# Kernel tuning notes

Measured on AMD Instinct MI355X. Metric: run time of the kernel, lower is better.

Reference implementation:

```python
import jax, jax.numpy as jnp
import numpy as np


def conv1x1(x, W, b):
    # x: [B, Cin, H, W], W: [Cout, Cin], b: [Cout] -> [B, Cout, H, W]
    return jnp.einsum('bchw,oc->bohw', x, W) + b[None, :, None, None]


def setup_inputs() -> dict:
    key = jax.random.key(0)
    ks = jax.random.split(key, 10)
    B, C, H, W = 16, 512, 64, 64
    c = C // 8  # in_ch // scale
    s_in = 1.0 / np.sqrt(C)
    s_c = 1.0 / np.sqrt(c)
    return {
        'x': jax.random.normal(ks[0], (B, C, H, W), dtype=jnp.float32),
        'Wq': jax.random.normal(ks[1], (c, C), dtype=jnp.float32) * s_in,
        'bq': jax.random.normal(ks[2], (c,), dtype=jnp.float32) * 0.01,
        'Wk': jax.random.normal(ks[3], (c, C), dtype=jnp.float32) * s_in,
        'bk': jax.random.normal(ks[4], (c,), dtype=jnp.float32) * 0.01,
        'Wv': jax.random.normal(ks[5], (c, C), dtype=jnp.float32) * s_in,
        'bv': jax.random.normal(ks[6], (c,), dtype=jnp.float32) * 0.01,
        'Wo': jax.random.normal(ks[7], (C, c), dtype=jnp.float32) * s_c,
        'bo': jax.random.normal(ks[8], (C,), dtype=jnp.float32) * 0.01,
        'gamma': jax.random.uniform(ks[9], (1,), dtype=jnp.float32),
    }


def reference(x, Wq, bq, Wk, bk, Wv, bv, Wo, bo, gamma):
    B, C, H, W = x.shape
    c = Wq.shape[0]
    N = H * W
    queries = conv1x1(x, Wq, bq).reshape(B, c, N)          # [B, c, N]
    # NOTE: original torch code does .view(-1, h*w, c): a pure reshape of the
    # contiguous [B, c, N] buffer, NOT a transpose. Reproduce exactly.
    keys = conv1x1(x, Wk, bk).reshape(B, N, c)             # [B, N, c] (reshape!)
    attn = jax.nn.softmax(jnp.einsum('bcn,bnd->bcd', queries, keys), axis=-1)  # [B, c, c]
    values = conv1x1(x, Wv, bv).reshape(B, c, N)           # [B, c, N]
    out = jnp.einsum('bcd,bdn->bcn', attn, values).reshape(B, c, H, W)
    out = conv1x1(out, Wo, bo)                             # [B, C, H, W]
    return out * gamma + x
```

## Files before the change

kernel.cpp:

```cpp
#include <hip/hip_runtime.h>

typedef unsigned short ushortT;
typedef unsigned int uintT;
typedef __attribute__((ext_vector_type(8))) short short8;
typedef __attribute__((ext_vector_type(4))) float float4v;

constexpr int B  = 16;
constexpr int C  = 512;
constexpr int CC = 64;
constexpr int N  = 4096;

constexpr size_t QK_OFF  = 0;
constexpr size_t S_OFF   = 8388608;
constexpr size_t VT_OFF  = 8454144;
constexpr size_t MF_OFF  = 10551296;
constexpr size_t WH_OFF  = 10813440;
constexpr size_t WL_OFF  = 10862592;
constexpr size_t WOT_OFF = 10911744;

#define GLL(lds, g) __builtin_amdgcn_global_load_lds( \
    (const __attribute__((address_space(1))) void*)(g), \
    (__attribute__((address_space(3))) void*)(lds), 16, 0, 0)

static __device__ __forceinline__ ushortT f2bf(float f) {
    uintT u = __float_as_uint(f);
    u = (u + 0x7fffu + ((u >> 16) & 1u)) >> 16;
    return (ushortT)u;
}
static __device__ __forceinline__ float bf2f(ushortT h) {
    return __uint_as_float(((uintT)h) << 16);
}

__global__ __launch_bounds__(256) void k_prep_w(
    const float* __restrict__ Wq, const float* __restrict__ Wk,
    const float* __restrict__ Wv, const float* __restrict__ Wo,
    ushortT* __restrict__ wh, ushortT* __restrict__ wl, float* __restrict__ wot)
{
    int idx = blockIdx.x * 256 + threadIdx.x;
    if (idx < 3 * CC * C) {
        int m = idx >> 9, k = idx & 511;
        const float* W = (m < 64) ? Wq : (m < 128 ? Wk : Wv);
        float v = W[(m & 63) * C + k];
        ushortT h = f2bf(v);
        ushortT l = f2bf(v - bf2f(h));
        int kt = k >> 6, kk = k & 63;
        size_t off = ((size_t)(kt * 192 + m)) * 64 + (size_t)(((kk >> 3) ^ (m & 7)) * 8) + (kk & 7);
        wh[off] = h;
        wl[off] = l;
    } else {
        int i2 = idx - 3 * CC * C;
        int cc = i2 >> 9, co = i2 & 511;
        wot[i2] = Wo[co * CC + cc];
    }
}

__global__ __launch_bounds__(256) void k_qkv(
    const float* __restrict__ x,
    const ushortT* __restrict__ wh, const ushortT* __restrict__ wl,
    const float* __restrict__ bq, const float* __restrict__ bk,
    const float* __restrict__ bv,
    float* __restrict__ qk, ushortT* __restrict__ vt)
{
    __shared__ ushortT As[192 * 64];
    __shared__ ushortT Bh[64 * 64];
    __shared__ ushortT Bl[64 * 64];

    const int tid  = threadIdx.x;
    const int n0   = blockIdx.x * 64;
    const int b    = blockIdx.y;
    const int lane = tid & 63;
    const int wv   = tid >> 6;
    const int L15  = lane & 15, Lq = lane >> 4;

    const int nl    = tid & 63;
    const int kbase = tid >> 6;

    float4v acc[3][4];
    const float4v vzero = {0.f, 0.f, 0.f, 0.f};
#pragma unroll
    for (int mi = 0; mi < 3; ++mi)
#pragma unroll
        for (int ni = 0; ni < 4; ++ni) acc[mi][ni] = vzero;

    for (int kt = 0; kt < 8; ++kt) {
        const float* xs = x + ((size_t)(b * C + kt * 64)) * N + n0 + nl;
#pragma unroll
        for (int it = 0; it < 16; ++it) {
            int kk = kbase + it * 4;
            float v = xs[(size_t)kk * N];
            ushortT h = f2bf(v);
            ushortT l = f2bf(v - bf2f(h));
            int idx = nl * 64 + (((kk >> 3) ^ (nl & 7)) * 8) + (kk & 7);
            Bh[idx] = h;
            Bl[idx] = l;
        }
        {
            const char* src = (const char*)wh + (size_t)kt * 24576;
#pragma unroll
            for (int i = 0; i < 6; ++i) {
                int off = i * 4096 + tid * 16;
                GLL((char*)As + off, src + off);
            }
        }
        __syncthreads();
#pragma unroll
        for (int s = 0; s < 2; ++s) {
            short8 fbh[4], fbl[4];
#pragma unroll
            for (int ni = 0; ni < 4; ++ni) {
                int row = ni * 16 + L15;
                int off = row * 64 + ((4 * s + Lq) ^ (row & 7)) * 8;
                fbh[ni] = *(const short8*)&Bh[off];
                fbl[ni] = *(const short8*)&Bl[off];
            }
#pragma unroll
            for (int mi = 0; mi < 3; ++mi) {
                int rm = 48 * wv + mi * 16 + L15;
                short8 a = *(const short8*)&As[rm * 64 + (((4 * s + Lq) ^ (rm & 7)) * 8)];
#pragma unroll
                for (int ni = 0; ni < 4; ++ni)
                    acc[mi][ni] = __builtin_amdgcn_mfma_f32_16x16x32_bf16(a, fbh[ni], acc[mi][ni], 0, 0, 0);
#pragma unroll
                for (int ni = 0; ni < 4; ++ni)
                    acc[mi][ni] = __builtin_amdgcn_mfma_f32_16x16x32_bf16(a, fbl[ni], acc[mi][ni], 0, 0, 0);
            }
        }
        __syncthreads();
        {
            const char* src = (const char*)wl + (size_t)kt * 24576;
#pragma unroll
            for (int i = 0; i < 6; ++i) {
                int off = i * 4096 + tid * 16;
                GLL((char*)As + off, src + off);
            }
        }
        __syncthreads();
#pragma unroll
        for (int s = 0; s < 2; ++s) {
            short8 fbh[4];
#pragma unroll
            for (int ni = 0; ni < 4; ++ni) {
                int row = ni * 16 + L15;
                fbh[ni] = *(const short8*)&Bh[row * 64 + ((4 * s + Lq) ^ (row & 7)) * 8];
            }
#pragma unroll
            for (int mi = 0; mi < 3; ++mi) {
                int rm = 48 * wv + mi * 16 + L15;
                short8 a = *(const short8*)&As[rm * 64 + (((4 * s + Lq) ^ (rm & 7)) * 8)];
#pragma unroll
                for (int ni = 0; ni < 4; ++ni)
                    acc[mi][ni] = __builtin_amdgcn_mfma_f32_16x16x32_bf16(a, fbh[ni], acc[mi][ni], 0, 0, 0);
            }
        }
        __syncthreads();
    }

#pragma unroll
    for (int mi = 0; mi < 3; ++mi) {
        int rbase = 48 * wv + mi * 16;
        int type = rbase >> 6;
#pragma unroll
        for (int ni = 0; ni < 4; ++ni) {
            int col = n0 + ni * 16 + L15;
            float4v v4 = acc[mi][ni];
#pragma unroll
            for (int reg = 0; reg < 4; ++reg) {
                int rl = (rbase + Lq * 4 + reg) & 63;
                float val = v4[reg];
                if (type == 0) {
                    qk[((size_t)(b * 64 + rl)) * N + col] = val + bq[rl];
                } else if (type == 1) {
                    qk[((size_t)((16 + b) * 64 + rl)) * N + col] = val + bk[rl];
                } else {
                    ushortT bb = f2bf(val + bv[rl]);
                    size_t off = ((size_t)(b * N + col)) * 64 + (((rl >> 3) ^ (col & 7)) * 8) + (rl & 7);
                    vt[off] = bb;
                }
            }
        }
    }
}

__global__ __launch_bounds__(256) void k_logits(
    const float* __restrict__ qk, float* __restrict__ S)
{
    int b  = blockIdx.x;
    int n0 = blockIdx.y * 64;
    __shared__ float Qs[64 * 68];
    __shared__ float Ks[64 * 64];

    const float* Qb = qk + (size_t)b * (CC * N);
    const float* Kb = qk + (size_t)(16 + b) * (CC * N);
    int tid = threadIdx.x;

    for (int t = tid; t < 64 * 64; t += 256) {
        int i = t >> 6, nn = t & 63;
        Qs[i * 68 + nn] = Qb[(size_t)i * N + n0 + nn];
        Ks[t] = Kb[(size_t)n0 * 64 + t];
    }
    __syncthreads();

    int ti = tid >> 4, tj = tid & 15;
    int i0 = ti * 4, j0 = tj * 4;
    float accl[4][4] = {};
    for (int nn = 0; nn < 64; ++nn) {
        float4 kv = *reinterpret_cast<const float4*>(&Ks[nn * 64 + j0]);
        float qa[4];
#pragma unroll
        for (int a = 0; a < 4; ++a) qa[a] = Qs[(i0 + a) * 68 + nn];
#pragma unroll
        for (int a = 0; a < 4; ++a) {
            accl[a][0] = fmaf(qa[a], kv.x, accl[a][0]);
            accl[a][1] = fmaf(qa[a], kv.y, accl[a][1]);
            accl[a][2] = fmaf(qa[a], kv.z, accl[a][2]);
            accl[a][3] = fmaf(qa[a], kv.w, accl[a][3]);
        }
    }
    float* Sb = S + b * (CC * CC);
#pragma unroll
    for (int a = 0; a < 4; ++a)
#pragma unroll
        for (int bb = 0; bb < 4; ++bb)
            atomicAdd(&Sb[(i0 + a) * 64 + j0 + bb], accl[a][bb]);
}

__global__ __launch_bounds__(256) void k_softmax_m(
    const float* __restrict__ S, const float* __restrict__ wot,
    ushortT* __restrict__ mf)
{
    int b = blockIdx.x, chunk = blockIdx.y;
    __shared__ float A[64 * 65];
    int tid = threadIdx.x;
    const float* Sb = S + b * (CC * CC);

    for (int t = tid; t < 4096; t += 256) A[(t >> 6) * 65 + (t & 63)] = Sb[t];
    __syncthreads();
    if (tid < 64) {
        float mx = -1e30f;
        for (int j = 0; j < 64; ++j) mx = fmaxf(mx, A[tid * 65 + j]);
        float sum = 0.f;
        for (int j = 0; j < 64; ++j) {
            float e = __expf(A[tid * 65 + j] - mx);
            A[tid * 65 + j] = e;
            sum += e;
        }
        float inv = 1.f / sum;
        for (int j = 0; j < 64; ++j) A[tid * 65 + j] *= inv;
    }
    __syncthreads();

    int co = chunk * 64 + (tid & 63);
    int e0 = (tid >> 6) * 16;
    float acc[16] = {};
    for (int cc = 0; cc < 64; ++cc) {
        float w = wot[cc * C + co];
#pragma unroll
        for (int ee = 0; ee < 16; ++ee)
            acc[ee] = fmaf(w, A[cc * 65 + e0 + ee], acc[ee]);
    }
#pragma unroll
    for (int d = 0; d < 2; ++d) {
        int c = (e0 >> 3) + d;
        uintT p0 = (uintT)f2bf(acc[d * 8 + 0]) | ((uintT)f2bf(acc[d * 8 + 1]) << 16);
        uintT p1 = (uintT)f2bf(acc[d * 8 + 2]) | ((uintT)f2bf(acc[d * 8 + 3]) << 16);
        uintT p2 = (uintT)f2bf(acc[d * 8 + 4]) | ((uintT)f2bf(acc[d * 8 + 5]) << 16);
        uintT p3 = (uintT)f2bf(acc[d * 8 + 6]) | ((uintT)f2bf(acc[d * 8 + 7]) << 16);
        uint4 pk = make_uint4(p0, p1, p2, p3);
        size_t off = ((size_t)(b * C + co)) * 64 + (size_t)((c ^ (co & 7)) * 8);
        *(uint4*)&mf[off] = pk;
    }
}

__global__ __launch_bounds__(256) void k_out(
    const ushortT* __restrict__ vt, const ushortT* __restrict__ mf,
    const float* __restrict__ x, const float* __restrict__ bo,
    const float* __restrict__ gamma, float* __restrict__ out)
{
    __shared__ ushortT As[64 * 64];
    __shared__ ushortT Bs[256 * 64];

    int b = blockIdx.x, ct = blockIdx.y, nt = blockIdx.z;
    int co0 = ct * 64, n0 = nt * 256;
    int tid = threadIdx.x;
    const char* asrc = (const char*)mf + ((size_t)(b * C + co0)) * 128;
    const char* bsrc = (const char*)vt + ((size_t)(b * N + n0)) * 128;
#pragma unroll
    for (int i = 0; i < 2; ++i) {
        int off = i * 4096 + tid * 16;
        GLL((char*)As + off, asrc + off);
    }
#pragma unroll
    for (int i = 0; i < 8; ++i) {
        int off = i * 4096 + tid * 16;
        GLL((char*)Bs + off, bsrc + off);
    }
    __syncthreads();

    int lane = tid & 63, wv = tid >> 6;
    int L15 = lane & 15, Lq = lane >> 4;
    float4v acc[4][4];
    const float4v vzero = {0.f, 0.f, 0.f, 0.f};
#pragma unroll
    for (int mi = 0; mi < 4; ++mi)
#pragma unroll
        for (int ni = 0; ni < 4; ++ni) acc[mi][ni] = vzero;

#pragma unroll
    for (int s = 0; s < 2; ++s) {
        short8 fb[4];
#pragma unroll
        for (int ni = 0; ni < 4; ++ni) {
            int row = wv * 64 + ni * 16 + L15;
            fb[ni] = *(const short8*)&Bs[row * 64 + ((4 * s + Lq) ^ (row & 7)) * 8];
        }
#pragma unroll
        for (int mi = 0; mi < 4; ++mi) {
            int rm = mi * 16 + L15;
            short8 a = *(const short8*)&As[rm * 64 + ((4 * s + Lq) ^ (rm & 7)) * 8];
#pragma unroll
            for (int ni = 0; ni < 4; ++ni)
                acc[mi][ni] = __builtin_amdgcn_mfma_f32_16x16x32_bf16(a, fb[ni], acc[mi][ni], 0, 0, 0);
        }
    }

    float g = gamma[0];
#pragma unroll
    for (int mi = 0; mi < 4; ++mi) {
        int cob = co0 + mi * 16 + Lq * 4;
#pragma unroll
        for (int ni = 0; ni < 4; ++ni) {
            int col = n0 + wv * 64 + ni * 16 + L15;
            float4v v4 = acc[mi][ni];
#pragma unroll
            for (int reg = 0; reg < 4; ++reg) {
                int c2 = cob + reg;
                size_t idx = ((size_t)(b * C + c2)) * N + col;
                out[idx] = fmaf(g, v4[reg] + bo[c2], x[idx]);
            }
        }
    }
}

extern "C" void kernel_launch(void* const* d_in, const int* in_sizes, int n_in,
                              void* d_out, int out_size, void* d_ws, size_t ws_size,
                              hipStream_t stream)
{
    const float* x     = (const float*)d_in[0];
    const float* Wq    = (const float*)d_in[1];
    const float* bq    = (const float*)d_in[2];
    const float* Wk    = (const float*)d_in[3];
    const float* bk    = (const float*)d_in[4];
    const float* Wv    = (const float*)d_in[5];
    const float* bv    = (const float*)d_in[6];
    const float* Wo    = (const float*)d_in[7];
    const float* bo    = (const float*)d_in[8];
    const float* gamma = (const float*)d_in[9];

    float* ws   = (float*)d_ws;
    float* qk   = ws + QK_OFF;
    float* S    = ws + S_OFF;
    ushortT* vt = (ushortT*)(ws + VT_OFF);
    ushortT* mf = (ushortT*)(ws + MF_OFF);
    ushortT* wh = (ushortT*)(ws + WH_OFF);
    ushortT* wl = (ushortT*)(ws + WL_OFF);
    float* wot  = ws + WOT_OFF;

    hipMemsetAsync(S, 0, (size_t)B * CC * CC * sizeof(float), stream);
    k_prep_w<<<512, 256, 0, stream>>>(Wq, Wk, Wv, Wo, wh, wl, wot);
    k_qkv<<<dim3(64, 16), 256, 0, stream>>>(x, wh, wl, bq, bk, bv, qk, vt);
    k_logits<<<dim3(16, 64), 256, 0, stream>>>(qk, S);
    k_softmax_m<<<dim3(16, 8), 256, 0, stream>>>(S, wot, mf);
    k_out<<<dim3(16, 8, 16), 256, 0, stream>>>(vt, mf, x, bo, gamma, (float*)d_out);
}
```

Measured before the change: 420.0 us.

## Double-buffer QKV projection, coarsen logits blocks, vectorize output epilogues

The QKV projection kernel now keeps the high and low weight halves in LDS together and double-buffers the split x tile. It prefetches the next k-tile's x into registers while the current tile runs its MFMAs, and merges the two MFMA passes into one loop with a single barrier pair. The logits kernel processes four N-chunks per block with float4 loads, which cuts atomic traffic by a factor of four, and the V store is packed into 4-element vectors. The output kernel swaps the MFMA operand roles so each lane holds contiguous spatial elements, enabling float4 loads of x and float4 stores of out. These changes cost extra LDS and registers per block, which may lower occupancy.

```diff
diff --git a/kernel.cpp b/kernel.cpp
--- a/kernel.cpp
+++ b/kernel.cpp
@@ -3,6 +3,7 @@
 typedef unsigned short ushortT;
 typedef unsigned int uintT;
 typedef __attribute__((ext_vector_type(8))) short short8;
+typedef __attribute__((ext_vector_type(4))) short short4v;
 typedef __attribute__((ext_vector_type(4))) float float4v;
 
 constexpr int B  = 16;
@@ -61,9 +62,10 @@
     const float* __restrict__ bv,
     float* __restrict__ qk, ushortT* __restrict__ vt)
 {
-    __shared__ ushortT As[192 * 64];
-    __shared__ ushortT Bh[64 * 64];
-    __shared__ ushortT Bl[64 * 64];
+    __shared__ ushortT Ah[192 * 64];
+    __shared__ ushortT Al[192 * 64];
+    __shared__ ushortT Bh[2][64 * 64];
+    __shared__ ushortT Bl[2][64 * 64];
 
     const int tid  = threadIdx.x;
     const int n0   = blockIdx.x * 64;
@@ -72,9 +74,12 @@
     const int wv   = tid >> 6;
     const int L15  = lane & 15, Lq = lane >> 4;
 
-    const int nl    = tid & 63;
-    const int kbase = tid >> 6;
-
+    const int nl  = tid & 63;
+    const int kg0 = tid >> 6;
+
+    const float* xb = x + (size_t)b * C * N + n0 + nl;
+
+    float xr[2][8];
     float4v acc[3][4];
     const float4v vzero = {0.f, 0.f, 0.f, 0.f};
 #pragma unroll
@@ -82,27 +87,51 @@
 #pragma unroll
         for (int ni = 0; ni < 4; ++ni) acc[mi][ni] = vzero;
 
+#pragma unroll
+    for (int u = 0; u < 2; ++u) {
+        const int kg = kg0 + 4 * u;
+#pragma unroll
+        for (int j = 0; j < 8; ++j)
+            xr[u][j] = xb[(size_t)(kg * 8 + j) * N];
+    }
+    {
+        const char* srcH = (const char*)wh;
+        const char* srcL = (const char*)wl;
+#pragma unroll
+        for (int i = 0; i < 6; ++i) {
+            int off = i * 4096 + tid * 16;
+            GLL((char*)Ah + off, srcH + off);
+            GLL((char*)Al + off, srcL + off);
+        }
+    }
+#pragma unroll
+    for (int u = 0; u < 2; ++u) {
+        const int kg = kg0 + 4 * u;
+        short8 h8, l8;
+#pragma unroll
+        for (int j = 0; j < 8; ++j) {
+            float v = xr[u][j];
+            ushortT h = f2bf(v);
+            h8[j] = (short)h;
+            l8[j] = (short)f2bf(v - bf2f(h));
+        }
+        int idx = nl * 64 + (kg ^ (nl & 7)) * 8;
+        *(short8*)&Bh[0][idx] = h8;
+        *(short8*)&Bl[0][idx] = l8;
+    }
+    __syncthreads();
+
     for (int kt = 0; kt < 8; ++kt) {
-        const float* xs = x + ((size_t)(b * C + kt * 64)) * N + n0 + nl;
-#pragma unroll
-        for (int it = 0; it < 16; ++it) {
-            int kk = kbase + it * 4;
-            float v = xs[(size_t)kk * N];
-            ushortT h = f2bf(v);
-            ushortT l = f2bf(v - bf2f(h));
-            int idx = nl * 64 + (((kk >> 3) ^ (nl & 7)) * 8) + (kk & 7);
-            Bh[idx] = h;
-            Bl[idx] = l;
-        }
-        {
-            const char* src = (const char*)wh + (size_t)kt * 24576;
-#pragma unroll
-            for (int i = 0; i < 6; ++i) {
-                int off = i * 4096 + tid * 16;
-                GLL((char*)As + off, src + off);
-            }
-        }
-        __syncthreads();
+        const int cur = kt & 1;
+        if (kt < 7) {
+#pragma unroll
+            for (int u = 0; u < 2; ++u) {
+                const int kg = kg0 + 4 * u;
+#pragma unroll
+                for (int j = 0; j < 8; ++j)
+                    xr[u][j] = xb[(size_t)((kt + 1) * 64 + kg * 8 + j) * N];
+            }
+        }
 #pragma unroll
         for (int s = 0; s < 2; ++s) {
             short8 fbh[4], fbl[4];
@@ -110,49 +139,54 @@
             for (int ni = 0; ni < 4; ++ni) {
                 int row = ni * 16 + L15;
                 int off = row * 64 + ((4 * s + Lq) ^ (row & 7)) * 8;
-                fbh[ni] = *(const short8*)&Bh[off];
-                fbl[ni] = *(const short8*)&Bl[off];
+                fbh[ni] = *(const short8*)&Bh[cur][off];
+                fbl[ni] = *(const short8*)&Bl[cur][off];
             }
 #pragma unroll
             for (int mi = 0; mi < 3; ++mi) {
                 int rm = 48 * wv + mi * 16 + L15;
-                short8 a = *(const short8*)&As[rm * 64 + (((4 * s + Lq) ^ (rm & 7)) * 8)];
+                int aoff = rm * 64 + ((4 * s + Lq) ^ (rm & 7)) * 8;
+                short8 ah = *(const short8*)&Ah[aoff];
+                short8 al = *(const short8*)&Al[aoff];
 #pragma unroll
                 for (int ni = 0; ni < 4; ++ni)
-                    acc[mi][ni] = __builtin_amdgcn_mfma_f32_16x16x32_bf16(a, fbh[ni], acc[mi][ni], 0, 0, 0);
+                    acc[mi][ni] = __builtin_amdgcn_mfma_f32_16x16x32_bf16(ah, fbh[ni], acc[mi][ni], 0, 0, 0);
 #pragma unroll
                 for (int ni = 0; ni < 4; ++ni)
-                    acc[mi][ni] = __builtin_amdgcn_mfma_f32_16x16x32_bf16(a, fbl[ni], acc[mi][ni], 0, 0, 0);
+                    acc[mi][ni] = __builtin_amdgcn_mfma_f32_16x16x32_bf16(al, fbh[ni], acc[mi][ni], 0, 0, 0);
+#pragma unroll
+                for (int ni = 0; ni < 4; ++ni)
+                    acc[mi][ni] = __builtin_amdgcn_mfma_f32_16x16x32_bf16(ah, fbl[ni], acc[mi][ni], 0, 0, 0);
             }
         }
         __syncthreads();
-        {
-            const char* src = (const char*)wl + (size_t)kt * 24576;
+        if (kt < 7) {
+            const char* srcH = (const char*)wh + (size_t)(kt + 1) * 24576;
+            const char* srcL = (const char*)wl + (size_t)(kt + 1) * 24576;
 #pragma unroll
             for (int i = 0; i < 6; ++i) {
                 int off = i * 4096 + tid * 16;
-                GLL((char*)As + off, src + off);
-            }
-        }
-        __syncthreads();
-#pragma unroll
-        for (int s = 0; s < 2; ++s) {
-            short8 fbh[4];
-#pragma unroll
-            for (int ni = 0; ni < 4; ++ni) {
-                int row = ni * 16 + L15;
-                fbh[ni] = *(const short8*)&Bh[row * 64 + ((4 * s + Lq) ^ (row & 7)) * 8];
-            }
-#pragma unroll
-            for (int mi = 0; mi < 3; ++mi) {
-                int rm = 48 * wv + mi * 16 + L15;
-                short8 a = *(const short8*)&As[rm * 64 + (((4 * s + Lq) ^ (rm & 7)) * 8)];
-#pragma unroll
-                for (int ni = 0; ni < 4; ++ni)
-                    acc[mi][ni] = __builtin_amdgcn_mfma_f32_16x16x32_bf16(a, fbh[ni], acc[mi][ni], 0, 0, 0);
-            }
-        }
-        __syncthreads();
+                GLL((char*)Ah + off, srcH + off);
+                GLL((char*)Al + off, srcL + off);
+            }
+            const int nxt = cur ^ 1;
+#pragma unroll
+            for (int u = 0; u < 2; ++u) {
+                const int kg = kg0 + 4 * u;
+                short8 h8, l8;
+#pragma unroll
+                for (int j = 0; j < 8; ++j) {
+                    float v = xr[u][j];
+                    ushortT h = f2bf(v);
+                    h8[j] = (short)h;
+                    l8[j] = (short)f2bf(v - bf2f(h));
+                }
+                int idx = nl * 64 + (kg ^ (nl & 7)) * 8;
+                *(short8*)&Bh[nxt][idx] = h8;
+                *(short8*)&Bl[nxt][idx] = l8;
+            }
+            __syncthreads();
+        }
     }
 
 #pragma unroll
@@ -163,19 +197,26 @@
         for (int ni = 0; ni < 4; ++ni) {
             int col = n0 + ni * 16 + L15;
             float4v v4 = acc[mi][ni];
-#pragma unroll
-            for (int reg = 0; reg < 4; ++reg) {
-                int rl = (rbase + Lq * 4 + reg) & 63;
-                float val = v4[reg];
-                if (type == 0) {
-                    qk[((size_t)(b * 64 + rl)) * N + col] = val + bq[rl];
-                } else if (type == 1) {
-                    qk[((size_t)((16 + b) * 64 + rl)) * N + col] = val + bk[rl];
-                } else {
-                    ushortT bb = f2bf(val + bv[rl]);
-                    size_t off = ((size_t)(b * N + col)) * 64 + (((rl >> 3) ^ (col & 7)) * 8) + (rl & 7);
-                    vt[off] = bb;
+            if (type == 0) {
+#pragma unroll
+                for (int reg = 0; reg < 4; ++reg) {
+                    int rl = (rbase + Lq * 4 + reg) & 63;
+                    qk[((size_t)(b * 64 + rl)) * N + col] = v4[reg] + bq[rl];
                 }
+            } else if (type == 1) {
+#pragma unroll
+                for (int reg = 0; reg < 4; ++reg) {
+                    int rl = (rbase + Lq * 4 + reg) & 63;
+                    qk[((size_t)((16 + b) * 64 + rl)) * N + col] = v4[reg] + bk[rl];
+                }
+            } else {
+                int rl0 = (rbase + Lq * 4) & 63;
+                short4v p;
+#pragma unroll
+                for (int reg = 0; reg < 4; ++reg)
+                    p[reg] = (short)f2bf(v4[reg] + bv[rl0 + reg]);
+                size_t off = ((size_t)(b * N + col)) * 64 + (size_t)(((rl0 >> 3) ^ (col & 7)) * 8) + (rl0 & 7);
+                *(short4v*)&vt[off] = p;
             }
         }
     }
@@ -184,36 +225,38 @@
 __global__ __launch_bounds__(256) void k_logits(
     const float* __restrict__ qk, float* __restrict__ S)
 {
-    int b  = blockIdx.x;
-    int n0 = blockIdx.y * 64;
+    int b = blockIdx.x;
     __shared__ float Qs[64 * 68];
     __shared__ float Ks[64 * 64];
 
     const float* Qb = qk + (size_t)b * (CC * N);
     const float* Kb = qk + (size_t)(16 + b) * (CC * N);
     int tid = threadIdx.x;
-
-    for (int t = tid; t < 64 * 64; t += 256) {
-        int i = t >> 6, nn = t & 63;
-        Qs[i * 68 + nn] = Qb[(size_t)i * N + n0 + nn];
-        Ks[t] = Kb[(size_t)n0 * 64 + t];
-    }
-    __syncthreads();
-
     int ti = tid >> 4, tj = tid & 15;
     int i0 = ti * 4, j0 = tj * 4;
     float accl[4][4] = {};
-    for (int nn = 0; nn < 64; ++nn) {
-        float4 kv = *reinterpret_cast<const float4*>(&Ks[nn * 64 + j0]);
-        float qa[4];
-#pragma unroll
-        for (int a = 0; a < 4; ++a) qa[a] = Qs[(i0 + a) * 68 + nn];
-#pragma unroll
-        for (int a = 0; a < 4; ++a) {
-            accl[a][0] = fmaf(qa[a], kv.x, accl[a][0]);
-            accl[a][1] = fmaf(qa[a], kv.y, accl[a][1]);
-            accl[a][2] = fmaf(qa[a], kv.z, accl[a][2]);
-            accl[a][3] = fmaf(qa[a], kv.w, accl[a][3]);
+
+    for (int ci = 0; ci < 4; ++ci) {
+        int n0 = (blockIdx.y * 4 + ci) * 64;
+        if (ci) __syncthreads();
+        for (int t = tid; t < 1024; t += 256) {
+            int i = t >> 4, c4 = (t & 15) * 4;
+            *(float4*)&Qs[i * 68 + c4] = *(const float4*)&Qb[(size_t)i * N + n0 + c4];
+            *(float4*)&Ks[t * 4]       = *(const float4*)&Kb[(size_t)n0 * 64 + t * 4];
+        }
+        __syncthreads();
+        for (int nn = 0; nn < 64; ++nn) {
+            float4 kv = *reinterpret_cast<const float4*>(&Ks[nn * 64 + j0]);
+            float qa[4];
+#pragma unroll
+            for (int a = 0; a < 4; ++a) qa[a] = Qs[(i0 + a) * 68 + nn];
+#pragma unroll
+            for (int a = 0; a < 4; ++a) {
+                accl[a][0] = fmaf(qa[a], kv.x, accl[a][0]);
+                accl[a][1] = fmaf(qa[a], kv.y, accl[a][1]);
+                accl[a][2] = fmaf(qa[a], kv.z, accl[a][2]);
+                accl[a][3] = fmaf(qa[a], kv.w, accl[a][3]);
+            }
         }
     }
     float* Sb = S + b * (CC * CC);
@@ -307,36 +350,41 @@
 
 #pragma unroll
     for (int s = 0; s < 2; ++s) {
-        short8 fb[4];
+        short8 fa[4], fbm[4];
+#pragma unroll
+        for (int mi = 0; mi < 4; ++mi) {
+            int row = wv * 64 + mi * 16 + L15;
+            fa[mi] = *(const short8*)&Bs[row * 64 + ((4 * s + Lq) ^ (row & 7)) * 8];
+        }
 #pragma unroll
         for (int ni = 0; ni < 4; ++ni) {
-            int row = wv * 64 + ni * 16 + L15;
-            fb[ni] = *(const short8*)&Bs[row * 64 + ((4 * s + Lq) ^ (row & 7)) * 8];
-        }
+            int rm = ni * 16 + L15;
+            fbm[ni] = *(const short8*)&As[rm * 64 + ((4 * s + Lq) ^ (rm & 7)) * 8];
+        }
+#pragma unroll
+        for (int mi = 0; mi < 4; ++mi)
+#pragma unroll
+            for (int ni = 0; ni < 4; ++ni)
+                acc[mi][ni] = __builtin_amdgcn_mfma_f32_16x16x32_bf16(fa[mi], fbm[ni], acc[mi][ni], 0, 0, 0);
+    }
+
+    float g = gamma[0];
+#pragma unroll
+    for (int ni = 0; ni < 4; ++ni) {
+        int co = co0 + ni * 16 + L15;
+        float bov = bo[co];
 #pragma unroll
         for (int mi = 0; mi < 4; ++mi) {
-            int rm = mi * 16 + L15;
-            short8 a = *(const short8*)&As[rm * 64 + ((4 * s + Lq) ^ (rm & 7)) * 8];
-#pragma unroll
-            for (int ni = 0; ni < 4; ++ni)
-                acc[mi][ni] = __builtin_amdgcn_mfma_f32_16x16x32_bf16(a, fb[ni], acc[mi][ni], 0, 0, 0);
-        }
-    }
-
-    float g = gamma[0];
-#pragma unroll
-    for (int mi = 0; mi < 4; ++mi) {
-        int cob = co0 + mi * 16 + Lq * 4;
-#pragma unroll
-        for (int ni = 0; ni < 4; ++ni) {
-            int col = n0 + wv * 64 + ni * 16 + L15;
+            int nbase = n0 + wv * 64 + mi * 16 + Lq * 4;
+            size_t idx = ((size_t)(b * C + co)) * N + nbase;
+            float4 xv = *(const float4*)&x[idx];
             float4v v4 = acc[mi][ni];
-#pragma unroll
-            for (int reg = 0; reg < 4; ++reg) {
-                int c2 = cob + reg;
-                size_t idx = ((size_t)(b * C + c2)) * N + col;
-                out[idx] = fmaf(g, v4[reg] + bo[c2], x[idx]);
-            }
+            float4 o;
+            o.x = fmaf(g, v4[0] + bov, xv.x);
+            o.y = fmaf(g, v4[1] + bov, xv.y);
+            o.z = fmaf(g, v4[2] + bov, xv.z);
+            o.w = fmaf(g, v4[3] + bov, xv.w);
+            *(float4*)&out[idx] = o;
         }
     }
 }
@@ -368,7 +416,7 @@
     hipMemsetAsync(S, 0, (size_t)B * CC * CC * sizeof(float), stream);
     k_prep_w<<<512, 256, 0, stream>>>(Wq, Wk, Wv, Wo, wh, wl, wot);
     k_qkv<<<dim3(64, 16), 256, 0, stream>>>(x, wh, wl, bq, bk, bv, qk, vt);
-    k_logits<<<dim3(16, 64), 256, 0, stream>>>(qk, S);
+    k_logits<<<dim3(16, 16), 256, 0, stream>>>(qk, S);
     k_softmax_m<<<dim3(16, 8), 256, 0, stream>>>(S, wot, mf);
     k_out<<<dim3(16, 8, 16), 256, 0, stream>>>(vt, mf, x, bo, gamma, (float*)d_out);
 }
```

Measured after the change: 374.2 us. -10.9%, faster.
